# Optimization experiments

Hardware: AMD Instinct MI355X
Metric: run time of the kernel (lower is better)

## Reference

```python
import jax, jax.numpy as jnp
import numpy as np

HEAD_SIZE = 64

def setup_inputs() -> dict:
    key = jax.random.key(0)
    k1, k2, k3, k4 = jax.random.split(key, 4)
    B, T, C, H = 8, 2048, 1024, HEAD_SIZE
    x = jax.random.normal(k1, (B, T, C), dtype=jnp.float32)
    attention_mask = jnp.ones((B, T), dtype=jnp.int32)
    # nn.Linear(C, H, bias=False): store as [C, H] so y = x @ W
    s = 1.0 / np.sqrt(C)
    Wk = jax.random.normal(k2, (C, H), dtype=jnp.float32) * s
    Wq = jax.random.normal(k3, (C, H), dtype=jnp.float32) * s
    Wv = jax.random.normal(k4, (C, H), dtype=jnp.float32) * s
    return {"x": x, "attention_mask": attention_mask, "Wk": Wk, "Wq": Wq, "Wv": Wv}

def reference(x, attention_mask, Wk, Wq, Wv):
    # x: [B, T, C]; projections -> [B, T, H]
    k = jnp.einsum('btc,ch->bth', x, Wk)
    q = jnp.einsum('btc,ch->bth', x, Wq)
    v = jnp.einsum('btc,ch->bth', x, Wv)
    scale = k.shape[-1] ** -0.5
    wei = jnp.einsum('bqh,bkh->bqk', q, k) * scale  # [B, T, T]
    mask = attention_mask[:, None, :]               # [B, 1, T] key-padding mask
    wei = jnp.where(mask == 0, -jnp.inf, wei)
    wei_soft = jax.nn.softmax(wei, axis=-1)
    # dropout p=0.0 (eval mode): identity
    out = jnp.einsum('bqk,bkh->bqh', wei_soft, v)   # [B, T, H]
    return out
```

## Files before the change

kernel.cpp:

```cpp
#include <hip/hip_runtime.h>
#include <hip/hip_bf16.h>

typedef __bf16 bf16;
typedef __bf16 bf16x4 __attribute__((ext_vector_type(4)));
typedef __bf16 bf16x8 __attribute__((ext_vector_type(8)));
typedef float f32x4 __attribute__((ext_vector_type(4)));

#define NB 8
#define NT 2048
#define NC 1024
#define NH 64

__device__ inline f32x4 zero4() {
    f32x4 z; z[0] = 0.f; z[1] = 0.f; z[2] = 0.f; z[3] = 0.f; return z;
}

__global__ __launch_bounds__(256) void pack_w(const float* __restrict__ Wq,
                                              const float* __restrict__ Wk,
                                              const float* __restrict__ Wv,
                                              bf16* __restrict__ Wt2) {
    const int g = blockIdx.x * 256 + threadIdx.x;
    const int l = g & 63;
    const int kc = (g >> 6) & 1;
    const int kt = (g >> 7) & 15;
    const int nf = g >> 11;
    const int n = nf * 16 + (l & 15);
    const int k0 = kt * 64 + kc * 32 + (l >> 4) * 8;
    const float* W = (n < 64) ? Wq : (n < 128) ? Wk : Wv;
    const int h = n & 63;
    bf16x8 o;
#pragma unroll
    for (int e = 0; e < 8; ++e) o[e] = (bf16)W[(k0 + e) * NH + h];
    *reinterpret_cast<bf16x8*>(Wt2 + (size_t)g * 8) = o;
}

__global__ __launch_bounds__(256, 2) void qkv_gemm(const float* __restrict__ x,
                                                   const bf16* __restrict__ Wt2,
                                                   bf16* __restrict__ qp,
                                                   bf16* __restrict__ kp2,
                                                   bf16* __restrict__ vt2) {
    __shared__ bf16 xs[2][64][72];
    const int tid = threadIdx.x;
    const int wave = tid >> 6, lane = tid & 63;
    const int l16 = lane & 15, lhi = lane >> 4;
    const int qh = wave & 1;
    const int ch = wave >> 1;
    const int row0 = blockIdx.x * 64;
    const bf16* wb = Wt2 + (size_t)ch * 98304 + lane * 8;

    f32x4 acc[2][6];
#pragma unroll
    for (int mr = 0; mr < 2; ++mr)
#pragma unroll
        for (int nf = 0; nf < 6; ++nf) acc[mr][nf] = zero4();

    const int sr = tid >> 4;
    const int sc = (tid & 15) * 4;

    float4 xv[3][4];
    bf16x8 bfr[2][12];

#define LOAD_X(SLOT, KT)  do { \
    _Pragma("unroll") for (int _i = 0; _i < 4; ++_i) \
        xv[SLOT][_i] = *reinterpret_cast<const float4*>( \
            &x[(size_t)(row0 + sr + _i * 16) * NC + (KT) * 64 + sc]); \
} while (0)

#define LOAD_B(SLOT, KT)  do { \
    _Pragma("unroll") for (int _nf = 0; _nf < 6; ++_nf) \
        _Pragma("unroll") for (int _kc = 0; _kc < 2; ++_kc) \
            bfr[SLOT][_nf * 2 + _kc] = *reinterpret_cast<const bf16x8*>( \
                wb + _nf * 16384 + (KT) * 1024 + _kc * 512); \
} while (0)

#define WRITE_XS(BUF, SLOT)  do { \
    _Pragma("unroll") for (int _i = 0; _i < 4; ++_i) { \
        bf16x4 _w; \
        _w[0] = (bf16)xv[SLOT][_i].x; _w[1] = (bf16)xv[SLOT][_i].y; \
        _w[2] = (bf16)xv[SLOT][_i].z; _w[3] = (bf16)xv[SLOT][_i].w; \
        *reinterpret_cast<bf16x4*>(&xs[BUF][sr + _i * 16][sc]) = _w; \
    } \
} while (0)

    LOAD_X(0, 0);
    LOAD_X(1, 1);
    LOAD_X(2, 2);
    LOAD_B(0, 0);
    WRITE_XS(0, 0);
    __syncthreads();

#pragma unroll
    for (int kt = 0; kt < 16; ++kt) {
        const int cur = kt & 1, nxt = cur ^ 1;
        if (kt < 13) LOAD_X(kt % 3, kt + 3);
        bf16x8 a[2][2];
#pragma unroll
        for (int mr = 0; mr < 2; ++mr)
#pragma unroll
            for (int kc = 0; kc < 2; ++kc)
                a[mr][kc] = *reinterpret_cast<const bf16x8*>(
                    &xs[cur][qh * 32 + mr * 16 + l16][kc * 32 + lhi * 8]);
        if (kt < 15) WRITE_XS(nxt, (kt + 1) % 3);
        if (kt < 15) LOAD_B(nxt, kt + 1);
        __syncthreads();
        __builtin_amdgcn_s_setprio(1);
#pragma unroll
        for (int nf = 0; nf < 6; ++nf)
#pragma unroll
            for (int kc = 0; kc < 2; ++kc)
#pragma unroll
                for (int mr = 0; mr < 2; ++mr)
                    acc[mr][nf] = __builtin_amdgcn_mfma_f32_16x16x32_bf16(
                        a[mr][kc], bfr[cur][nf * 2 + kc], acc[mr][nf], 0, 0, 0);
        __builtin_amdgcn_s_setprio(0);
    }
#undef LOAD_X
#undef LOAD_B
#undef WRITE_XS

#pragma unroll
    for (int mr = 0; mr < 2; ++mr)
#pragma unroll
    for (int nf = 0; nf < 6; ++nf) {
        const int col = ch * 96 + nf * 16 + l16;
#pragma unroll
        for (int r = 0; r < 4; ++r) {
            const int row = row0 + qh * 32 + mr * 16 + lhi * 4 + r;
            const bf16 val = (bf16)acc[mr][nf][r];
            const int bb = row >> 11, kv = row & (NT - 1);
            const int t = kv >> 6;
            if (col < 64) {
                qp[(size_t)row * NH + col] = val;
            } else if (col < 128) {
                const int h = col - 64;
                const int kvb = (kv >> 4) & 3;
                const int lK = ((h & 31) >> 3) * 16 + (kv & 15);
                kp2[((((size_t)(bb * 32 + t) * 4 + kvb) * 2 + (h >> 5)) * 64 + lK) * 8 + (h & 7)] = val;
            } else {
                const int h = col - 128;
                const int kcV = (kv >> 5) & 1;
                const int lV = ((kv & 31) >> 3) * 16 + (h & 15);
                vt2[((((size_t)(bb * 32 + t) * 2 + kcV) * 4 + (h >> 4)) * 64 + lV) * 8 + (kv & 7)] = val;
            }
        }
    }
}

__global__ __launch_bounds__(256, 2) void attn(const bf16* __restrict__ qp,
                                               const bf16* __restrict__ kp2,
                                               const bf16* __restrict__ vt2,
                                               const int* __restrict__ mask,
                                               float* __restrict__ out) {
    __shared__ __align__(16) char smem[4 * 2 * 16 * 68 * 4];
    bf16 (*p_lds)[64][20] = reinterpret_cast<bf16 (*)[64][20]>(smem);
    float (*sm_o)[2][16][68] = reinterpret_cast<float (*)[2][16][68]>(smem);
    __shared__ float sm_m[4][2][16], sm_l[4][2][16];

    const int tid = threadIdx.x;
    const int sp = tid >> 6, lane = tid & 63;
    const int l16 = lane & 15, lhi = lane >> 4;
    const int b = blockIdx.y;
    const int tb = sp * 8;
    bf16* const pw = &p_lds[sp][0][0];

    bf16x8 aq[2][2];
#pragma unroll
    for (int t = 0; t < 2; ++t)
#pragma unroll
        for (int hc = 0; hc < 2; ++hc)
            aq[t][hc] = *reinterpret_cast<const bf16x8*>(
                &qp[((size_t)b * NT + blockIdx.x * 32 + t * 16 + l16) * NH + hc * 32 + lhi * 8]);

    const bf16* kw = kp2 + (size_t)b * 131072 + (size_t)tb * 4096 + lane * 8;
    const bf16* vw = vt2 + (size_t)b * 131072 + (size_t)tb * 4096 + lane * 8;
    const int*  mw = mask + b * NT + tb * 64 + lhi * 4;

    float m[2] = {-1e30f, -1e30f}, l[2] = {0.f, 0.f};
    f32x4 o[2][4];
#pragma unroll
    for (int t = 0; t < 2; ++t)
#pragma unroll
        for (int hb = 0; hb < 4; ++hb) o[t][hb] = zero4();

#pragma unroll
    for (int it = 0; it < 8; ++it) {
        const int fo = it * 4096;
        bf16x8 kf[8];
#pragma unroll
        for (int i = 0; i < 8; ++i)
            kf[i] = *reinterpret_cast<const bf16x8*>(kw + fo + i * 512);
        int4 mv[4];
#pragma unroll
        for (int kvb = 0; kvb < 4; ++kvb)
            mv[kvb] = *reinterpret_cast<const int4*>(mw + it * 64 + kvb * 16);
        f32x4 s[2][4];
        __builtin_amdgcn_s_setprio(1);
#pragma unroll
        for (int t = 0; t < 2; ++t)
#pragma unroll
            for (int kvb = 0; kvb < 4; ++kvb) {
                s[t][kvb] = zero4();
                s[t][kvb] = __builtin_amdgcn_mfma_f32_16x16x32_bf16(kf[kvb * 2], aq[t][0], s[t][kvb], 0, 0, 0);
                s[t][kvb] = __builtin_amdgcn_mfma_f32_16x16x32_bf16(kf[kvb * 2 + 1], aq[t][1], s[t][kvb], 0, 0, 0);
            }
        __builtin_amdgcn_s_setprio(0);
        bf16x8 vf[8];
#pragma unroll
        for (int i = 0; i < 8; ++i)
            vf[i] = *reinterpret_cast<const bf16x8*>(vw + fo + i * 512);
#pragma unroll
        for (int t = 0; t < 2; ++t)
#pragma unroll
            for (int kvb = 0; kvb < 4; ++kvb) {
                s[t][kvb][0] = mv[kvb].x ? s[t][kvb][0] * 0.125f : -1e30f;
                s[t][kvb][1] = mv[kvb].y ? s[t][kvb][1] * 0.125f : -1e30f;
                s[t][kvb][2] = mv[kvb].z ? s[t][kvb][2] * 0.125f : -1e30f;
                s[t][kvb][3] = mv[kvb].w ? s[t][kvb][3] * 0.125f : -1e30f;
            }
#pragma unroll
        for (int t = 0; t < 2; ++t) {
            float tm = s[t][0][0];
#pragma unroll
            for (int kvb = 0; kvb < 4; ++kvb)
#pragma unroll
                for (int r = 0; r < 4; ++r) tm = fmaxf(tm, s[t][kvb][r]);
            tm = fmaxf(tm, __shfl_xor(tm, 16));
            tm = fmaxf(tm, __shfl_xor(tm, 32));
            const float mn = fmaxf(m[t], tm);
            const float alpha = __expf(m[t] - mn);
            m[t] = mn;
            float ps = 0.f;
#pragma unroll
            for (int kvb = 0; kvb < 4; ++kvb)
#pragma unroll
                for (int r = 0; r < 4; ++r) {
                    const float p = __expf(s[t][kvb][r] - m[t]);
                    s[t][kvb][r] = p;
                    ps += p;
                }
            ps += __shfl_xor(ps, 16);
            ps += __shfl_xor(ps, 32);
            l[t] = l[t] * alpha + ps;
#pragma unroll
            for (int kvb = 0; kvb < 4; ++kvb) {
                bf16x4 w;
                w[0] = (bf16)s[t][kvb][0]; w[1] = (bf16)s[t][kvb][1];
                w[2] = (bf16)s[t][kvb][2]; w[3] = (bf16)s[t][kvb][3];
                const int row = l16 + 16 * ((kvb * 2 + (lhi >> 1)) & 3);
                *reinterpret_cast<bf16x4*>(pw + row * 20 + (kvb >> 1) * 8 + (lhi & 1) * 4) = w;
            }
            float ar[4];
#pragma unroll
            for (int r = 0; r < 4; ++r) ar[r] = __shfl(alpha, lhi * 4 + r);
#pragma unroll
            for (int hb = 0; hb < 4; ++hb)
#pragma unroll
                for (int r = 0; r < 4; ++r) o[t][hb][r] *= ar[r];
            __builtin_amdgcn_s_setprio(1);
#pragma unroll
            for (int kc = 0; kc < 2; ++kc) {
                const bf16* pr = pw + lane * 20 + kc * 8;
                const bf16x4 lo = *reinterpret_cast<const bf16x4*>(pr);
                const bf16x4 hi = *reinterpret_cast<const bf16x4*>(pr + 4);
                const bf16x8 pa = __builtin_shufflevector(lo, hi, 0, 1, 2, 3, 4, 5, 6, 7);
#pragma unroll
                for (int hb = 0; hb < 4; ++hb)
                    o[t][hb] = __builtin_amdgcn_mfma_f32_16x16x32_bf16(pa, vf[kc * 4 + hb], o[t][hb], 0, 0, 0);
            }
            __builtin_amdgcn_s_setprio(0);
        }
    }

    __syncthreads();
#pragma unroll
    for (int t = 0; t < 2; ++t) {
#pragma unroll
        for (int hb = 0; hb < 4; ++hb)
#pragma unroll
            for (int r = 0; r < 4; ++r)
                sm_o[sp][t][lhi * 4 + r][hb * 16 + l16] = o[t][hb][r];
        if (lhi == 0) {
            sm_m[sp][t][l16] = m[t];
            sm_l[sp][t][l16] = l[t];
        }
    }
    __syncthreads();

#pragma unroll
    for (int e = 0; e < 8; ++e) {
        const int idx = e * 256 + tid;
        const int row = idx >> 6;
        const int col = idx & 63;
        const int t2 = row >> 4, r16 = row & 15;
        float M = sm_m[0][t2][r16];
#pragma unroll
        for (int s2 = 1; s2 < 4; ++s2) M = fmaxf(M, sm_m[s2][t2][r16]);
        float L = 0.f, accv = 0.f;
#pragma unroll
        for (int s2 = 0; s2 < 4; ++s2) {
            const float w = __expf(sm_m[s2][t2][r16] - M);
            L += w * sm_l[s2][t2][r16];
            accv += w * sm_o[s2][t2][r16][col];
        }
        out[((size_t)b * NT + blockIdx.x * 32 + row) * NH + col] = accv / L;
    }
}

extern "C" void kernel_launch(void* const* d_in, const int* in_sizes, int n_in,
                              void* d_out, int out_size, void* d_ws, size_t ws_size,
                              hipStream_t stream) {
    const float* x    = (const float*)d_in[0];
    const int*   mask = (const int*)d_in[1];
    const float* Wk   = (const float*)d_in[2];
    const float* Wq   = (const float*)d_in[3];
    const float* Wv   = (const float*)d_in[4];
    float* out = (float*)d_out;

    char* ws = (char*)d_ws;
    bf16* Wt2 = (bf16*)(ws);
    bf16* qp  = (bf16*)(ws + (512 << 10));
    bf16* kp2 = (bf16*)(ws + (512 << 10) + (2 << 20));
    bf16* vt2 = (bf16*)(ws + (512 << 10) + (4 << 20));

    pack_w<<<dim3(96), dim3(256), 0, stream>>>(Wq, Wk, Wv, Wt2);
    qkv_gemm<<<dim3(256), dim3(256), 0, stream>>>(x, Wt2, qp, kp2, vt2);
    attn<<<dim3(64, 8), dim3(256), 0, stream>>>(qp, kp2, vt2, mask, out);
}
```

Before: 48.10 us.

## Double query rows per attention block and fold scale into Wq with exp2

Each attention block now processes 64 query rows instead of 32, so every K/V fragment loaded from global memory is reused across four 16-row tiles, and the grid is halved. The softmax scale and log2(e) are folded into the packed Wq weights so the kernel can use exp2 directly, and masking becomes an additive bias. A lazy rescale skips the running-max update unless the new max exceeds the old by more than 8 (in log2 units). The trade-offs are higher register pressure and fewer blocks (256 total), which may reduce occupancy and latency hiding.

Result: slower. 58.30 us (+21.2%).

```diff
diff --git a/kernel.cpp b/kernel.cpp
--- a/kernel.cpp
+++ b/kernel.cpp
@@ -10,6 +10,8 @@
 #define NT 2048
 #define NC 1024
 #define NH 64
+
+#define QSCALE 0.18033688011112042f
 
 __device__ inline f32x4 zero4() {
     f32x4 z; z[0] = 0.f; z[1] = 0.f; z[2] = 0.f; z[3] = 0.f; return z;
@@ -27,10 +29,11 @@
     const int n = nf * 16 + (l & 15);
     const int k0 = kt * 64 + kc * 32 + (l >> 4) * 8;
     const float* W = (n < 64) ? Wq : (n < 128) ? Wk : Wv;
+    const float sc = (n < 64) ? QSCALE : 1.0f;
     const int h = n & 63;
     bf16x8 o;
 #pragma unroll
-    for (int e = 0; e < 8; ++e) o[e] = (bf16)W[(k0 + e) * NH + h];
+    for (int e = 0; e < 8; ++e) o[e] = (bf16)(W[(k0 + e) * NH + h] * sc);
     *reinterpret_cast<bf16x8*>(Wt2 + (size_t)g * 8) = o;
 }
 
@@ -151,34 +154,35 @@
                                                const bf16* __restrict__ vt2,
                                                const int* __restrict__ mask,
                                                float* __restrict__ out) {
-    __shared__ __align__(16) char smem[4 * 2 * 16 * 68 * 4];
+    __shared__ __align__(16) char smem[4 * 4 * 16 * 68 * 4];
     bf16 (*p_lds)[64][20] = reinterpret_cast<bf16 (*)[64][20]>(smem);
-    float (*sm_o)[2][16][68] = reinterpret_cast<float (*)[2][16][68]>(smem);
-    __shared__ float sm_m[4][2][16], sm_l[4][2][16];
+    float (*sm_o)[4][16][68] = reinterpret_cast<float (*)[4][16][68]>(smem);
+    __shared__ float sm_m[4][4][16], sm_l[4][4][16];
 
     const int tid = threadIdx.x;
     const int sp = tid >> 6, lane = tid & 63;
     const int l16 = lane & 15, lhi = lane >> 4;
     const int b = blockIdx.y;
+    const int q_base = blockIdx.x * 64;
     const int tb = sp * 8;
     bf16* const pw = &p_lds[sp][0][0];
 
-    bf16x8 aq[2][2];
-#pragma unroll
-    for (int t = 0; t < 2; ++t)
+    bf16x8 aq[4][2];
+#pragma unroll
+    for (int t = 0; t < 4; ++t)
 #pragma unroll
         for (int hc = 0; hc < 2; ++hc)
             aq[t][hc] = *reinterpret_cast<const bf16x8*>(
-                &qp[((size_t)b * NT + blockIdx.x * 32 + t * 16 + l16) * NH + hc * 32 + lhi * 8]);
+                &qp[((size_t)b * NT + q_base + t * 16 + l16) * NH + hc * 32 + lhi * 8]);
 
     const bf16* kw = kp2 + (size_t)b * 131072 + (size_t)tb * 4096 + lane * 8;
     const bf16* vw = vt2 + (size_t)b * 131072 + (size_t)tb * 4096 + lane * 8;
     const int*  mw = mask + b * NT + tb * 64 + lhi * 4;
 
-    float m[2] = {-1e30f, -1e30f}, l[2] = {0.f, 0.f};
-    f32x4 o[2][4];
-#pragma unroll
-    for (int t = 0; t < 2; ++t)
+    float m[4] = {-1e30f, -1e30f, -1e30f, -1e30f}, l[4] = {0.f, 0.f, 0.f, 0.f};
+    f32x4 o[4][4];
+#pragma unroll
+    for (int t = 0; t < 4; ++t)
 #pragma unroll
         for (int hb = 0; hb < 4; ++hb) o[t][hb] = zero4();
 
@@ -193,69 +197,72 @@
 #pragma unroll
         for (int kvb = 0; kvb < 4; ++kvb)
             mv[kvb] = *reinterpret_cast<const int4*>(mw + it * 64 + kvb * 16);
-        f32x4 s[2][4];
-        __builtin_amdgcn_s_setprio(1);
-#pragma unroll
-        for (int t = 0; t < 2; ++t)
-#pragma unroll
-            for (int kvb = 0; kvb < 4; ++kvb) {
-                s[t][kvb] = zero4();
-                s[t][kvb] = __builtin_amdgcn_mfma_f32_16x16x32_bf16(kf[kvb * 2], aq[t][0], s[t][kvb], 0, 0, 0);
-                s[t][kvb] = __builtin_amdgcn_mfma_f32_16x16x32_bf16(kf[kvb * 2 + 1], aq[t][1], s[t][kvb], 0, 0, 0);
-            }
-        __builtin_amdgcn_s_setprio(0);
         bf16x8 vf[8];
 #pragma unroll
         for (int i = 0; i < 8; ++i)
             vf[i] = *reinterpret_cast<const bf16x8*>(vw + fo + i * 512);
-#pragma unroll
-        for (int t = 0; t < 2; ++t)
+        f32x4 bias[4];
+#pragma unroll
+        for (int kvb = 0; kvb < 4; ++kvb) {
+            bias[kvb][0] = mv[kvb].x ? 0.f : -1e30f;
+            bias[kvb][1] = mv[kvb].y ? 0.f : -1e30f;
+            bias[kvb][2] = mv[kvb].z ? 0.f : -1e30f;
+            bias[kvb][3] = mv[kvb].w ? 0.f : -1e30f;
+        }
+
+#pragma unroll
+        for (int t = 0; t < 4; ++t) {
+            f32x4 s[4];
+            __builtin_amdgcn_s_setprio(1);
 #pragma unroll
             for (int kvb = 0; kvb < 4; ++kvb) {
-                s[t][kvb][0] = mv[kvb].x ? s[t][kvb][0] * 0.125f : -1e30f;
-                s[t][kvb][1] = mv[kvb].y ? s[t][kvb][1] * 0.125f : -1e30f;
-                s[t][kvb][2] = mv[kvb].z ? s[t][kvb][2] * 0.125f : -1e30f;
-                s[t][kvb][3] = mv[kvb].w ? s[t][kvb][3] * 0.125f : -1e30f;
-            }
-#pragma unroll
-        for (int t = 0; t < 2; ++t) {
-            float tm = s[t][0][0];
+                s[kvb] = zero4();
+                s[kvb] = __builtin_amdgcn_mfma_f32_16x16x32_bf16(kf[kvb * 2], aq[t][0], s[kvb], 0, 0, 0);
+                s[kvb] = __builtin_amdgcn_mfma_f32_16x16x32_bf16(kf[kvb * 2 + 1], aq[t][1], s[kvb], 0, 0, 0);
+            }
+            __builtin_amdgcn_s_setprio(0);
+#pragma unroll
+            for (int kvb = 0; kvb < 4; ++kvb) s[kvb] += bias[kvb];
+            float tm = s[0][0];
 #pragma unroll
             for (int kvb = 0; kvb < 4; ++kvb)
 #pragma unroll
-                for (int r = 0; r < 4; ++r) tm = fmaxf(tm, s[t][kvb][r]);
+                for (int r = 0; r < 4; ++r) tm = fmaxf(tm, s[kvb][r]);
             tm = fmaxf(tm, __shfl_xor(tm, 16));
             tm = fmaxf(tm, __shfl_xor(tm, 32));
-            const float mn = fmaxf(m[t], tm);
-            const float alpha = __expf(m[t] - mn);
-            m[t] = mn;
+            if (!__all(tm <= m[t] + 8.f)) {
+                const float mn = fmaxf(m[t], tm);
+                const float alpha = __builtin_exp2f(m[t] - mn);
+                m[t] = mn;
+                l[t] *= alpha;
+                float ar[4];
+#pragma unroll
+                for (int r = 0; r < 4; ++r) ar[r] = __shfl(alpha, lhi * 4 + r);
+#pragma unroll
+                for (int hb = 0; hb < 4; ++hb)
+#pragma unroll
+                    for (int r = 0; r < 4; ++r) o[t][hb][r] *= ar[r];
+            }
             float ps = 0.f;
 #pragma unroll
             for (int kvb = 0; kvb < 4; ++kvb)
 #pragma unroll
                 for (int r = 0; r < 4; ++r) {
-                    const float p = __expf(s[t][kvb][r] - m[t]);
-                    s[t][kvb][r] = p;
+                    const float p = __builtin_exp2f(s[kvb][r] - m[t]);
+                    s[kvb][r] = p;
                     ps += p;
                 }
             ps += __shfl_xor(ps, 16);
             ps += __shfl_xor(ps, 32);
-            l[t] = l[t] * alpha + ps;
+            l[t] += ps;
 #pragma unroll
             for (int kvb = 0; kvb < 4; ++kvb) {
                 bf16x4 w;
-                w[0] = (bf16)s[t][kvb][0]; w[1] = (bf16)s[t][kvb][1];
-                w[2] = (bf16)s[t][kvb][2]; w[3] = (bf16)s[t][kvb][3];
+                w[0] = (bf16)s[kvb][0]; w[1] = (bf16)s[kvb][1];
+                w[2] = (bf16)s[kvb][2]; w[3] = (bf16)s[kvb][3];
                 const int row = l16 + 16 * ((kvb * 2 + (lhi >> 1)) & 3);
                 *reinterpret_cast<bf16x4*>(pw + row * 20 + (kvb >> 1) * 8 + (lhi & 1) * 4) = w;
             }
-            float ar[4];
-#pragma unroll
-            for (int r = 0; r < 4; ++r) ar[r] = __shfl(alpha, lhi * 4 + r);
-#pragma unroll
-            for (int hb = 0; hb < 4; ++hb)
-#pragma unroll
-                for (int r = 0; r < 4; ++r) o[t][hb][r] *= ar[r];
             __builtin_amdgcn_s_setprio(1);
 #pragma unroll
             for (int kc = 0; kc < 2; ++kc) {
@@ -273,7 +280,7 @@
 
     __syncthreads();
 #pragma unroll
-    for (int t = 0; t < 2; ++t) {
+    for (int t = 0; t < 4; ++t) {
 #pragma unroll
         for (int hb = 0; hb < 4; ++hb)
 #pragma unroll
@@ -287,7 +294,7 @@
     __syncthreads();
 
 #pragma unroll
-    for (int e = 0; e < 8; ++e) {
+    for (int e = 0; e < 16; ++e) {
         const int idx = e * 256 + tid;
         const int row = idx >> 6;
         const int col = idx & 63;
@@ -298,11 +305,11 @@
         float L = 0.f, accv = 0.f;
 #pragma unroll
         for (int s2 = 0; s2 < 4; ++s2) {
-            const float w = __expf(sm_m[s2][t2][r16] - M);
+            const float w = __builtin_exp2f(sm_m[s2][t2][r16] - M);
             L += w * sm_l[s2][t2][r16];
             accv += w * sm_o[s2][t2][r16][col];
         }
-        out[((size_t)b * NT + blockIdx.x * 32 + row) * NH + col] = accv / L;
+        out[((size_t)b * NT + q_base + row) * NH + col] = accv / L;
     }
 }
 
@@ -324,5 +331,5 @@
 
     pack_w<<<dim3(96), dim3(256), 0, stream>>>(Wq, Wk, Wv, Wt2);
     qkv_gemm<<<dim3(256), dim3(256), 0, stream>>>(x, Wt2, qp, kp2, vt2);
-    attn<<<dim3(64, 8), dim3(256), 0, stream>>>(qp, kp2, vt2, mask, out);
-}
+    attn<<<dim3(32, 8), dim3(256), 0, stream>>>(qp, kp2, vt2, mask, out);
+}
```
